# Performance work log

Hardware: AMD Instinct MI355X
Metric: run time of the kernel (lower is better)

The kernel has to match this reference:

```python
import jax, jax.numpy as jnp
import numpy as np

STRIDES = (8, 16, 32)
SIZES = ((80, 80), (40, 40), (20, 20))  # 640x640 input
PRE_TOP_K = 1000
KEEP_TOP_K = 100
IOU_THR = 0.65
SCORE_THR = 0.25
CLASS_OFFSET = 4096.0  # > max image extent, for class-aware NMS


def setup_inputs() -> dict:
    key = jax.random.key(0)
    ks = jax.random.split(key, 6)
    B, C = 8, 1203
    d = {}
    for i, (h, w) in enumerate(SIZES):
        d[f"cls_scores_{i}"] = jax.random.normal(ks[i], (B, C, h, w), dtype=jnp.float32)
        d[f"bbox_preds_{i}"] = jax.random.uniform(ks[3 + i], (B, 4, h, w), dtype=jnp.float32)
    return d


def _flatten(feats, ch):
    B = feats[0].shape[0]
    return jnp.concatenate([f.transpose(0, 2, 3, 1).reshape(B, -1, ch) for f in feats], axis=1)


def _priors():
    pts, strs = [], []
    for (h, w), s in zip(SIZES, STRIDES):
        yy, xx = jnp.meshgrid(jnp.arange(h, dtype=jnp.float32), jnp.arange(w, dtype=jnp.float32), indexing="ij")
        pts.append(jnp.stack([(xx.ravel() + 0.5) * s, (yy.ravel() + 0.5) * s], axis=-1))
        strs.append(jnp.full((h * w,), float(s), dtype=jnp.float32))
    return jnp.concatenate(pts, 0), jnp.concatenate(strs, 0)


def _decode(priors, preds, stride):
    # DistancePointBBoxCoder: preds are LTRB distances scaled by stride.
    d = preds * stride[None, :, None]  # [B,N,4]
    x1 = priors[None, :, 0] - d[..., 0]
    y1 = priors[None, :, 1] - d[..., 1]
    x2 = priors[None, :, 0] + d[..., 2]
    y2 = priors[None, :, 1] + d[..., 3]
    return jnp.stack([x1, y1, x2, y2], axis=-1)


def _iou_matrix(b):
    area = (b[:, 2] - b[:, 0]) * (b[:, 3] - b[:, 1])
    lt = jnp.maximum(b[:, None, :2], b[None, :, :2])
    rb = jnp.minimum(b[:, None, 2:], b[None, :, 2:])
    wh = jnp.clip(rb - lt, 0.0)
    inter = wh[..., 0] * wh[..., 1]
    return inter / (area[:, None] + area[None, :] - inter + 1e-7)


def _nms_single(boxes, scores, labels):
    # boxes [N,4], scores [N] (max over classes), labels [N] int
    ts, idx = jax.lax.top_k(scores, PRE_TOP_K)
    b = boxes[idx]
    l = labels[idx]
    valid = ts > SCORE_THR
    off = b + (l.astype(b.dtype) * CLASS_OFFSET)[:, None]  # class-aware trick
    iou = _iou_matrix(off)  # [K,K]

    def body(keep, i):
        suppressed = jnp.any(keep & (iou[:, i] > IOU_THR))
        keep = keep.at[i].set(valid[i] & ~suppressed)
        return keep, None

    keep, _ = jax.lax.scan(body, jnp.zeros((PRE_TOP_K,), bool), jnp.arange(PRE_TOP_K))
    kept_scores = jnp.where(keep, ts, -1.0)
    fs, fi = jax.lax.top_k(kept_scores, KEEP_TOP_K)
    m = fs > 0.0
    det_boxes = jnp.where(m[:, None], b[fi], 0.0)
    det_scores = jnp.where(m, fs, 0.0)
    det_labels = jnp.where(m, l[fi], -1)
    num_dets = m.sum().astype(jnp.int32)
    return num_dets, det_boxes, det_scores, det_labels


def reference(cls_scores_0, cls_scores_1, cls_scores_2, bbox_preds_0, bbox_preds_1, bbox_preds_2):
    C = cls_scores_0.shape[1]
    cls_scores = jax.nn.sigmoid(_flatten([cls_scores_0, cls_scores_1, cls_scores_2], C))  # [B,N,C]
    preds = _flatten([bbox_preds_0, bbox_preds_1, bbox_preds_2], 4)  # [B,N,4]
    priors, stride = _priors()
    boxes = _decode(priors, preds, stride)  # [B,N,4]
    max_scores = cls_scores.max(axis=-1)  # [B,N]
    labels = cls_scores.argmax(axis=-1)  # [B,N]
    num_dets, det_boxes, det_scores, det_labels = jax.vmap(_nms_single)(boxes, max_scores, labels)
    return num_dets, det_boxes, det_scores, det_labels
```

## Files before the change

kernel.cpp:

```cpp
#include <hip/hip_runtime.h>
#include <math.h>

#pragma clang fp contract(off)

typedef unsigned long long u64;
typedef unsigned int u32;
typedef float f4 __attribute__((ext_vector_type(4)));
typedef unsigned long long u64x2 __attribute__((ext_vector_type(2)));

#define BB 8
#define CC_TOT 1203
#define NANC 8400
#define NSEG 8
#define SEGN 1050
#define NSEL 1000
#define NCAND 1024
#define NT 1024
#define NBATCH 128
#define NCHUNK_MAX 16

__device__ __forceinline__ u32 okey32(float v) {
  u32 b = __float_as_uint(v);
  return (b & 0x80000000u) ? ~b : (b | 0x80000000u);
}

__device__ __forceinline__ float unokey32(u32 ok) {
  u32 fb = (ok & 0x80000000u) ? (ok & 0x7FFFFFFFu) : ~ok;
  return __uint_as_float(fb);
}

__global__ __launch_bounds__(256) void kmax(const float* __restrict__ cls0,
                                            const float* __restrict__ cls1,
                                            const float* __restrict__ cls2,
                                            u64* __restrict__ part,
                                            int chunkSz, int nchunk) {
  int bx = blockIdx.x;
  int per = nchunk * BB;
  int tg = bx / per;
  int rem = bx - tg * per;
  int chunk = rem >> 3;
  int b = rem & 7;
  const float* cls; int hw4, aoff, col0;
  if (tg < 7)      { cls = cls0; hw4 = 1600; aoff = 0;    col0 = tg << 8; }
  else if (tg < 9) { cls = cls1; hw4 = 400;  aoff = 6400; col0 = (tg - 7) << 8; }
  else             { cls = cls2; hw4 = 100;  aoff = 8000; col0 = 0; }
  int col = col0 + (int)threadIdx.x;
  if (col >= hw4) return;
  int c0 = chunk * chunkSz;
  int c1 = c0 + chunkSz; if (c1 > CC_TOT) c1 = CC_TOT;

  const f4* base = (const f4*)cls + (size_t)b * CC_TOT * hw4 + col;
  f4 m = (f4){-3.4e38f, -3.4e38f, -3.4e38f, -3.4e38f};
  int ix0 = c0, ix1 = c0, ix2 = c0, ix3 = c0;

#define UPD(v, c)                                   \
  do {                                              \
    if ((v)[0] > m[0]) { m[0] = (v)[0]; ix0 = (c); } \
    if ((v)[1] > m[1]) { m[1] = (v)[1]; ix1 = (c); } \
    if ((v)[2] > m[2]) { m[2] = (v)[2]; ix2 = (c); } \
    if ((v)[3] > m[3]) { m[3] = (v)[3]; ix3 = (c); } \
  } while (0)

  int c = c0;
  for (; c + 8 <= c1; c += 8) {
    const f4* p = base + (size_t)c * hw4;
    f4 v0 = p[0];
    f4 v1 = p[(size_t)1 * hw4];
    f4 v2 = p[(size_t)2 * hw4];
    f4 v3 = p[(size_t)3 * hw4];
    f4 v4 = p[(size_t)4 * hw4];
    f4 v5 = p[(size_t)5 * hw4];
    f4 v6 = p[(size_t)6 * hw4];
    f4 v7 = p[(size_t)7 * hw4];
    UPD(v0, c + 0); UPD(v1, c + 1); UPD(v2, c + 2); UPD(v3, c + 3);
    UPD(v4, c + 4); UPD(v5, c + 5); UPD(v6, c + 6); UPD(v7, c + 7);
  }
  for (; c < c1; ++c) {
    f4 v = base[(size_t)c * hw4];
    UPD(v, c);
  }
#undef UPD

  u64* dst = part + ((size_t)chunk * BB + b) * NANC + aoff + (size_t)col * 4;
  u64x2 s01 = { ((u64)okey32(m[0]) << 32) | (u64)(u32)~(u32)ix0,
                ((u64)okey32(m[1]) << 32) | (u64)(u32)~(u32)ix1 };
  u64x2 s23 = { ((u64)okey32(m[2]) << 32) | (u64)(u32)~(u32)ix2,
                ((u64)okey32(m[3]) << 32) | (u64)(u32)~(u32)ix3 };
  *((u64x2*)dst)     = s01;
  *((u64x2*)dst + 1) = s23;
}

struct DecodeArrays {
  float xo1[NCAND], yo1[NCAND], xo2[NCAND], yo2[NCAND], ar[NCAND];
  float rx1[NCAND], ry1[NCAND], rx2[NCAND], ry2[NCAND], sc[NCAND];
  int lab[NCAND], val[NCAND];
};

__device__ __forceinline__ void hist_addc(u32* hist, u32 digit, int lane) {
  u64 peers = ~0ull;
  for (int bit = 0; bit < 13; ++bit) {
    u64 bal = __ballot((digit >> bit) & 1u);
    peers &= ((digit >> bit) & 1u) ? bal : ~bal;
  }
  int leader = __ffsll((unsigned long long)peers) - 1;
  if (digit < 4096u && lane == leader)
    atomicAdd(&hist[digit], (u32)__popcll((unsigned long long)peers));
}

__device__ __forceinline__ void suffix_pick(u32* hist, u32* waveTot, u32* waveSufExcl,
                                            u64* prefixSh, u32* rankSh, u32* binCntSh,
                                            u64 prefix, u32 rank, int shift,
                                            int tid, int lane, int wv) {
  u32 l0 = hist[4 * tid], l1 = hist[4 * tid + 1], l2 = hist[4 * tid + 2], l3 = hist[4 * tid + 3];
  u32 psum = l0 + l1 + l2 + l3;
  u32 x = psum;
  for (int s = 1; s < 64; s <<= 1) { u32 v = __shfl_down(x, s); if (lane + s < 64) x += v; }
  if (lane == 0) waveTot[wv] = x;
  __syncthreads();
  if (tid < 16) {
    u32 y = waveTot[tid]; u32 z = y;
    for (int s = 1; s < 16; s <<= 1) { u32 v = __shfl_down(z, s); if (tid + s < 16) z += v; }
    waveSufExcl[tid] = z - y;
  }
  __syncthreads();
  u32 S = x + waveSufExcl[wv];
  u32 G3 = S - psum; u32 G2 = G3 + l3; u32 G1 = G2 + l2; u32 G0 = G1 + l1;
  u32 r = rank;
  if      (G3 < r && G3 + l3 >= r) { *prefixSh = prefix | ((u64)(4u * tid + 3) << shift); *rankSh = r - G3; *binCntSh = l3; }
  else if (G2 < r && G2 + l2 >= r) { *prefixSh = prefix | ((u64)(4u * tid + 2) << shift); *rankSh = r - G2; *binCntSh = l2; }
  else if (G1 < r && G1 + l1 >= r) { *prefixSh = prefix | ((u64)(4u * tid + 1) << shift); *rankSh = r - G1; *binCntSh = l1; }
  else if (G0 < r && G0 + l0 >= r) { *prefixSh = prefix | ((u64)(4u * tid + 0) << shift); *rankSh = r - G0; *binCntSh = l0; }
}

__device__ __forceinline__ u64 select_after_hist(const u64* keys, int n, u32 target,
                                                 u32* hist, u32* waveTot, u32* waveSufExcl,
                                                 u64* prefixSh, u32* rankSh, u32* binCntSh,
                                                 int tid, int lane, int wv) {
  suffix_pick(hist, waveTot, waveSufExcl, prefixSh, rankSh, binCntSh,
              0ull, target, 52, tid, lane, wv);
  __syncthreads();
  u64 pfx = *prefixSh; u32 rk = *rankSh; u32 lc = *binCntSh;
  __syncthreads();
  if (lc == rk) return pfx;
  for (int pass = 2; pass >= 0; --pass) {
    int shift = 16 + pass * 12;
    for (int i = tid; i < 4096; i += NT) hist[i] = 0;
    __syncthreads();
    u64 hiMask = (~0ull) << (shift + 12);
    for (int i = tid; i < n; i += NT) {
      u64 k = keys[i];
      if ((k & hiMask) == (pfx & hiMask))
        atomicAdd(&hist[(u32)((k >> shift) & 4095u)], 1u);
    }
    __syncthreads();
    suffix_pick(hist, waveTot, waveSufExcl, prefixSh, rankSh, binCntSh,
                pfx, rk, shift, tid, lane, wv);
    __syncthreads();
    pfx = *prefixSh; rk = *rankSh; lc = *binCntSh;
    __syncthreads();
    if (lc == rk) break;
  }
  return pfx;
}

__device__ __forceinline__ void gather_ge(const u64* keys, int n, u64 K, u64* dst, u32* cnt,
                                          int tid, int lane, u32 bound) {
  for (int i = tid; i < n; i += NT) {
    u64 k = keys[i];
    bool sel = (k >= K);
    u64 mask = __ballot(sel);
    if (mask) {
      int leader = __ffsll((unsigned long long)mask) - 1;
      u32 basep = 0;
      if (lane == leader) basep = atomicAdd(cnt, (u32)__popcll((unsigned long long)mask));
      basep = __shfl((int)basep, leader);
      if (sel) {
        u32 pos = basep + (u32)__popcll((unsigned long long)(mask & ((1ull << lane) - 1ull)));
        if (pos < bound) dst[pos] = k;
      }
    }
  }
}

__global__ __launch_bounds__(1024) void kseg(const u64* __restrict__ part, int nchunk,
                                             u64* __restrict__ candSeg) {
  __shared__ __align__(16) u64 keys[SEGN];
  __shared__ u32 hist[4096];
  __shared__ u32 waveTot[16], waveSufExcl[16];
  __shared__ u64 prefixSh;
  __shared__ u32 rankSh, binCntSh, cnt;

  int seg = blockIdx.x >> 3;
  int b = blockIdx.x & 7;
  int tid = threadIdx.x, lane = tid & 63, wv = tid >> 6;
  int a0 = seg * SEGN;

  const u64x2* psrc = (const u64x2*)part + ((size_t)b * NANC + a0) / 2;
  const size_t PL2 = (size_t)BB * NANC / 2;

  for (int i = tid; i < 4096; i += NT) hist[i] = 0;
  if (tid == 0) cnt = 0;
  __syncthreads();

  {
    u32 d0 = 4096u, d1 = 4096u;
    if (tid < SEGN / 2) {
      u64x2 m = psrc[tid];
      int ch = 1;
      for (; ch + 4 <= nchunk; ch += 4) {
        u64x2 v0 = psrc[(size_t)(ch + 0) * PL2 + tid];
        u64x2 v1 = psrc[(size_t)(ch + 1) * PL2 + tid];
        u64x2 v2 = psrc[(size_t)(ch + 2) * PL2 + tid];
        u64x2 v3 = psrc[(size_t)(ch + 3) * PL2 + tid];
        u64 a01 = (v0[0] > v1[0]) ? v0[0] : v1[0];
        u64 a23 = (v2[0] > v3[0]) ? v2[0] : v3[0];
        u64 aa = (a01 > a23) ? a01 : a23;
        if (aa > m[0]) m[0] = aa;
        u64 b01 = (v0[1] > v1[1]) ? v0[1] : v1[1];
        u64 b23 = (v2[1] > v3[1]) ? v2[1] : v3[1];
        u64 bb2_ = (b01 > b23) ? b01 : b23;
        if (bb2_ > m[1]) m[1] = bb2_;
      }
      for (; ch < nchunk; ++ch) {
        u64x2 v = psrc[(size_t)ch * PL2 + tid];
        if (v[0] > m[0]) m[0] = v[0];
        if (v[1] > m[1]) m[1] = v[1];
      }
      u32 aA = (u32)(a0 + 2 * tid), aB = aA + 1;
      u64 k0 = (m[0] & 0xFFFFFFFF00000000ull) | ((u64)(0xFFFFu - aA) << 16) | (u64)(~(u32)m[0] & 0xFFFFu);
      u64 k1 = (m[1] & 0xFFFFFFFF00000000ull) | ((u64)(0xFFFFu - aB) << 16) | (u64)(~(u32)m[1] & 0xFFFFu);
      keys[2 * tid] = k0;
      keys[2 * tid + 1] = k1;
      d0 = (u32)(k0 >> 52);
      d1 = (u32)(k1 >> 52);
    }
    hist_addc(hist, d0, lane);
    hist_addc(hist, d1, lane);
  }
  __syncthreads();

  u64 K = select_after_hist(keys, SEGN, NBATCH, hist, waveTot, waveSufExcl,
                            &prefixSh, &rankSh, &binCntSh, tid, lane, wv);
  gather_ge(keys, SEGN, K, candSeg + ((size_t)b * NSEG + seg) * NBATCH, &cnt,
            tid, lane, NBATCH);
}

__device__ __forceinline__ void decode_into(DecodeArrays* d, int rk, u64 my, int b,
                                            const float* bb0, const float* bb1, const float* bb2) {
  int label = (int)(u32)(my & 0xFFFFull);
  int idx = 0xFFFF - (int)(u32)((my >> 16) & 0xFFFFull);
  float logit = unokey32((u32)(my >> 32));
  float sc = 1.0f / (1.0f + expf(-logit));

  int w, str, off, hwl; const float* bb;
  if (idx < 6400)      { w = 80; str = 8;  off = 0;    hwl = 6400; bb = bb0; }
  else if (idx < 8000) { w = 40; str = 16; off = 6400; hwl = 1600; bb = bb1; }
  else                 { w = 20; str = 32; off = 8000; hwl = 400;  bb = bb2; }
  int p = idx - off;
  int y = p / w;
  int x = p - y * w;
  float fs = (float)str;
  float px = ((float)x + 0.5f) * fs;
  float py = ((float)y + 0.5f) * fs;
  const float* bp = bb + (size_t)b * 4 * hwl + p;
  float t0 = bp[0] * fs;
  float t1 = bp[hwl] * fs;
  float t2 = bp[2 * hwl] * fs;
  float t3 = bp[3 * hwl] * fs;
  float x1 = px - t0, y1 = py - t1, x2 = px + t2, y2 = py + t3;
  float lo = (float)label * 4096.0f;
  float ox1 = x1 + lo, oy1 = y1 + lo, ox2 = x2 + lo, oy2 = y2 + lo;
  float area = (ox2 - ox1) * (oy2 - oy1);

  d->xo1[rk] = ox1; d->yo1[rk] = oy1; d->xo2[rk] = ox2; d->yo2[rk] = oy2; d->ar[rk] = area;
  d->rx1[rk] = x1;  d->ry1[rk] = y1;  d->rx2[rk] = x2;  d->ry2[rk] = y2;  d->sc[rk] = sc;
  d->lab[rk] = label;
  d->val[rk] = (sc > 0.25f) ? 1 : 0;
}

__device__ __forceinline__ int nms_pass(const DecodeArrays* d, int bound, int lane, int* outIdx) {
  float ax1 = 0, ay1 = 0, ax2 = 0, ay2 = 0, aar = 0; int aon = 0;
  float bx1 = 0, by1 = 0, bx2 = 0, by2 = 0, bar = 0; int bon = 0;
  int kept = 0;
  for (int i = 0; i < bound; ++i) {
    if (kept >= 100) break;
    float cx1 = d->xo1[i], cy1 = d->yo1[i], cx2 = d->xo2[i], cy2 = d->yo2[i], car = d->ar[i];
    bool sup = false;
    if (aon) {
      float ltx = fmaxf(ax1, cx1), lty = fmaxf(ay1, cy1);
      float rbx = fminf(ax2, cx2), rby = fminf(ay2, cy2);
      float wd = fmaxf(rbx - ltx, 0.0f), ht = fmaxf(rby - lty, 0.0f);
      float inter = wd * ht;
      sup = sup || ((inter / (aar + car - inter + 1e-7f)) > 0.65f);
    }
    if (bon) {
      float ltx = fmaxf(bx1, cx1), lty = fmaxf(by1, cy1);
      float rbx = fminf(bx2, cx2), rby = fminf(by2, cy2);
      float wd = fmaxf(rbx - ltx, 0.0f), ht = fmaxf(rby - lty, 0.0f);
      float inter = wd * ht;
      sup = sup || ((inter / (bar + car - inter + 1e-7f)) > 0.65f);
    }
    bool anysup = __any(sup);
    if (d->val[i] != 0 && !anysup) {
      if (kept < 64) {
        if (lane == kept) { ax1 = cx1; ay1 = cy1; ax2 = cx2; ay2 = cy2; aar = car; aon = 1; }
      } else {
        if (lane == kept - 64) { bx1 = cx1; by1 = cy1; bx2 = cx2; by2 = cy2; bar = car; bon = 1; }
      }
      if (lane == 0) outIdx[kept] = i;
      ++kept;
    }
  }
  return kept;
}

__global__ __launch_bounds__(1024) void kmerge(const u64* __restrict__ part, int nchunk,
                                               const u64* __restrict__ candSeg,
                                               const float* __restrict__ bb0,
                                               const float* __restrict__ bb1,
                                               const float* __restrict__ bb2,
                                               float* __restrict__ out) {
  __shared__ union ShU {
    u64 fk[NANC];
    DecodeArrays d;
  } sh;
  __shared__ u32 hist[4096];
  __shared__ u32 waveTot[16], waveSufExcl[16];
  __shared__ u64 prefixSh;
  __shared__ u32 rankSh, binCntSh;
  __shared__ u32 gcnt, aCnt;
  __shared__ __align__(16) u64 cand[NCAND];
  __shared__ __align__(16) u64 candA[NBATCH];
  __shared__ __align__(16) u32 cm[NBATCH * 4];
  __shared__ u64 VwSh[2];
  __shared__ int outIdx[128];
  __shared__ int keptSh;

  int b = blockIdx.x;
  int tid = threadIdx.x;
  int lane = tid & 63;
  int wv = tid >> 6;

  for (int i = tid; i < 4096; i += NT) hist[i] = 0;
  if (tid == 0) { gcnt = 0; aCnt = 0; }
  __syncthreads();
  u64 myk = candSeg[(size_t)b * (NSEG * NBATCH) + tid];
  cand[tid] = myk;
  hist_addc(hist, (u32)(myk >> 52), lane);
  if (tid < NBATCH * 4) cm[tid] = 0;
  __syncthreads();

  u64 K = select_after_hist(cand, NCAND, NBATCH, hist, waveTot, waveSufExcl,
                            &prefixSh, &rankSh, &binCntSh, tid, lane, wv);
  gather_ge(cand, NCAND, K, candA, &aCnt, tid, lane, NBATCH);
  __syncthreads();

  if (tid < NBATCH) {
    u64 my = candA[tid];
    int rk = 0;
    const u64x2* cav = (const u64x2*)candA;
    #pragma unroll
    for (int j2 = 0; j2 < NBATCH / 2; ++j2) {
      u64x2 p = cav[j2];
      rk += (p[0] > my) ? 1 : 0;
      rk += (p[1] > my) ? 1 : 0;
    }
    decode_into(&sh.d, rk, my, b, bb0, bb1, bb2);
  }
  __syncthreads();

  if (tid < NBATCH) {
    u64 bal = __ballot(sh.d.val[tid] != 0);
    if (lane == 0) VwSh[tid >> 6] = bal;
  }

  {
    int c = tid & 127;
    int g = tid >> 7;
    float cx1 = sh.d.xo1[c], cy1 = sh.d.yo1[c], cx2 = sh.d.xo2[c], cy2 = sh.d.yo2[c], car = sh.d.ar[c];
    u32 bits = 0;
    int j0 = g * 16;
    for (int jj = 0; jj < 16; ++jj) {
      int j = j0 + jj;
      float ltx = fmaxf(sh.d.xo1[j], cx1), lty = fmaxf(sh.d.yo1[j], cy1);
      float rbx = fminf(sh.d.xo2[j], cx2), rby = fminf(sh.d.yo2[j], cy2);
      float wd = fmaxf(rbx - ltx, 0.0f), ht = fmaxf(rby - lty, 0.0f);
      float inter = wd * ht;
      bool sup = (inter / (sh.d.ar[j] + car - inter + 1e-7f)) > 0.65f;
      bits |= sup ? (1u << jj) : 0u;
    }
    atomicOr(&cm[c * 4 + (g >> 1)], bits << ((g & 1) * 16));
  }
  __syncthreads();

  if (tid == 0) {
    u32 L0 = (u32)VwSh[0], L1 = (u32)(VwSh[0] >> 32);
    u32 L2 = (u32)VwSh[1], L3 = (u32)(VwSh[1] >> 32);
    int kept = 0;
    while (kept < 100) {
      int i;
      if (L0)      i = __ffs(L0) - 1;
      else if (L1) i = 31 + __ffs(L1);
      else if (L2) i = 63 + __ffs(L2);
      else if (L3) i = 95 + __ffs(L3);
      else break;
      outIdx[kept++] = i;
      const u32* c4 = &cm[i * 4];
      L0 &= ~c4[0]; L1 &= ~c4[1]; L2 &= ~c4[2]; L3 &= ~c4[3];
      if (i < 32)      L0 &= ~(1u << i);
      else if (i < 64) L1 &= ~(1u << (i - 32));
      else if (i < 96) L2 &= ~(1u << (i - 64));
      else             L3 &= ~(1u << (i - 96));
    }
    keptSh = kept;
  }
  __syncthreads();

  if (keptSh < 100) {
    const u64x2* psrc = (const u64x2*)(part + (size_t)b * NANC);
    const size_t PL2 = (size_t)BB * NANC / 2;
    for (int i = tid; i < 4096; i += NT) hist[i] = 0;
    __syncthreads();
    {
      u64x2* fdst = (u64x2*)sh.fk;
      for (int i = tid; i < NANC / 2; i += NT) {
        u64x2 m = psrc[i];
        for (int ch = 1; ch < nchunk; ++ch) {
          u64x2 v = psrc[(size_t)ch * PL2 + i];
          if (v[0] > m[0]) m[0] = v[0];
          if (v[1] > m[1]) m[1] = v[1];
        }
        u32 i0 = (u32)(2 * i), i1 = (u32)(2 * i + 1);
        u64x2 r;
        r[0] = (m[0] & 0xFFFFFFFF00000000ull) | ((u64)(0xFFFFu - i0) << 16) | (u64)(~(u32)m[0] & 0xFFFFu);
        r[1] = (m[1] & 0xFFFFFFFF00000000ull) | ((u64)(0xFFFFu - i1) << 16) | (u64)(~(u32)m[1] & 0xFFFFu);
        fdst[i] = r;
        hist_addc(hist, (u32)(r[0] >> 52), lane);
        hist_addc(hist, (u32)(r[1] >> 52), lane);
      }
    }
    __syncthreads();
    u64 Kf = select_after_hist(sh.fk, NANC, NSEL, hist, waveTot, waveSufExcl,
                               &prefixSh, &rankSh, &binCntSh, tid, lane, wv);
    gather_ge(sh.fk, NANC, Kf, cand, &gcnt, tid, lane, NSEL);
    __syncthreads();
    if (tid < NSEL) {
      u64 my = cand[tid];
      int rk = 0;
      const u64x2* cbv = (const u64x2*)cand;
      for (int j2 = 0; j2 < NSEL / 2; ++j2) {
        u64x2 p = cbv[j2];
        rk += (p[0] > my) ? 1 : 0;
        rk += (p[1] > my) ? 1 : 0;
      }
      decode_into(&sh.d, rk, my, b, bb0, bb1, bb2);
    }
    __syncthreads();
    if (tid < 64) {
      int kept = nms_pass(&sh.d, NSEL, lane, outIdx);
      if (lane == 0) keptSh = kept;
    }
    __syncthreads();
  }

  int kept = keptSh;
  float* o_nd = out;
  float* o_box = out + BB;
  float* o_sc = out + BB + BB * 100 * 4;
  float* o_lb = out + BB + BB * 100 * 4 + BB * 100;
  if (tid == 0) o_nd[b] = (float)kept;
  if (tid < 100) {
    int s = tid;
    float v0 = 0, v1 = 0, v2 = 0, v3 = 0, sv = 0, lv = -1.0f;
    if (s < kept) {
      int i = outIdx[s];
      v0 = sh.d.rx1[i]; v1 = sh.d.ry1[i]; v2 = sh.d.rx2[i]; v3 = sh.d.ry2[i];
      sv = sh.d.sc[i]; lv = (float)sh.d.lab[i];
    }
    float* bo = o_box + ((size_t)b * 100 + s) * 4;
    bo[0] = v0; bo[1] = v1; bo[2] = v2; bo[3] = v3;
    o_sc[b * 100 + s] = sv;
    o_lb[b * 100 + s] = lv;
  }
}

extern "C" void kernel_launch(void* const* d_in, const int* in_sizes, int n_in,
                              void* d_out, int out_size, void* d_ws, size_t ws_size,
                              hipStream_t stream) {
  const float* cls0 = (const float*)d_in[0];
  const float* bb0  = (const float*)d_in[1];
  const float* cls1 = (const float*)d_in[2];
  const float* bb1  = (const float*)d_in[3];
  const float* cls2 = (const float*)d_in[4];
  const float* bb2  = (const float*)d_in[5];

  size_t planeB = (size_t)BB * NANC * sizeof(u64);
  size_t candB = (size_t)BB * NSEG * NBATCH * sizeof(u64);
  u64* part = (u64*)d_ws;
  int nchunk = 1;
  if (ws_size > candB + planeB) {
    nchunk = (int)((ws_size - candB) / planeB);
    if (nchunk > NCHUNK_MAX) nchunk = NCHUNK_MAX;
    if (nchunk < 1) nchunk = 1;
  }
  int chunkSz = (CC_TOT + nchunk - 1) / nchunk;
  nchunk = (CC_TOT + chunkSz - 1) / chunkSz;
  u64* candSeg = part + (size_t)nchunk * BB * NANC;

  kmax<<<dim3(10 * nchunk * BB), dim3(256), 0, stream>>>(cls0, cls1, cls2, part, chunkSz, nchunk);
  kseg<<<dim3(NSEG * BB), dim3(NT), 0, stream>>>(part, nchunk, candSeg);
  kmerge<<<dim3(BB), dim3(NT), 0, stream>>>(part, nchunk, candSeg, bb0, bb1, bb2, (float*)d_out);
}
```

Measured before the change: 119.8 us.

## Fuse segment select and merge kernels via last-block atomic counter

Merges the per-segment top-k kernel and the per-batch merge/NMS kernel into one launch. Each segment block publishes its candidates, then increments a per-batch atomic counter, and the last block to arrive for a batch performs the merge, decode and NMS. This removes one kernel launch and its inter-kernel gap, at the cost of an extra memset, atomics, and fences. The segment blocks now declare the larger merge shared-memory footprint, which may reduce how many blocks fit per CU.

Result: slower. 148.5 us (+24.0%).

```diff
diff --git a/kernel.cpp b/kernel.cpp
--- a/kernel.cpp
+++ b/kernel.cpp
@@ -182,13 +182,98 @@
   }
 }
 
-__global__ __launch_bounds__(1024) void kseg(const u64* __restrict__ part, int nchunk,
-                                             u64* __restrict__ candSeg) {
-  __shared__ __align__(16) u64 keys[SEGN];
+__device__ __forceinline__ void decode_into(DecodeArrays* d, int rk, u64 my, int b,
+                                            const float* bb0, const float* bb1, const float* bb2) {
+  int label = (int)(u32)(my & 0xFFFFull);
+  int idx = 0xFFFF - (int)(u32)((my >> 16) & 0xFFFFull);
+  float logit = unokey32((u32)(my >> 32));
+  float sc = 1.0f / (1.0f + expf(-logit));
+
+  int w, str, off, hwl; const float* bb;
+  if (idx < 6400)      { w = 80; str = 8;  off = 0;    hwl = 6400; bb = bb0; }
+  else if (idx < 8000) { w = 40; str = 16; off = 6400; hwl = 1600; bb = bb1; }
+  else                 { w = 20; str = 32; off = 8000; hwl = 400;  bb = bb2; }
+  int p = idx - off;
+  int y = p / w;
+  int x = p - y * w;
+  float fs = (float)str;
+  float px = ((float)x + 0.5f) * fs;
+  float py = ((float)y + 0.5f) * fs;
+  const float* bp = bb + (size_t)b * 4 * hwl + p;
+  float t0 = bp[0] * fs;
+  float t1 = bp[hwl] * fs;
+  float t2 = bp[2 * hwl] * fs;
+  float t3 = bp[3 * hwl] * fs;
+  float x1 = px - t0, y1 = py - t1, x2 = px + t2, y2 = py + t3;
+  float lo = (float)label * 4096.0f;
+  float ox1 = x1 + lo, oy1 = y1 + lo, ox2 = x2 + lo, oy2 = y2 + lo;
+  float area = (ox2 - ox1) * (oy2 - oy1);
+
+  d->xo1[rk] = ox1; d->yo1[rk] = oy1; d->xo2[rk] = ox2; d->yo2[rk] = oy2; d->ar[rk] = area;
+  d->rx1[rk] = x1;  d->ry1[rk] = y1;  d->rx2[rk] = x2;  d->ry2[rk] = y2;  d->sc[rk] = sc;
+  d->lab[rk] = label;
+  d->val[rk] = (sc > 0.25f) ? 1 : 0;
+}
+
+__device__ __forceinline__ int nms_pass(const DecodeArrays* d, int bound, int lane, int* outIdx) {
+  float ax1 = 0, ay1 = 0, ax2 = 0, ay2 = 0, aar = 0; int aon = 0;
+  float bx1 = 0, by1 = 0, bx2 = 0, by2 = 0, bar = 0; int bon = 0;
+  int kept = 0;
+  for (int i = 0; i < bound; ++i) {
+    if (kept >= 100) break;
+    float cx1 = d->xo1[i], cy1 = d->yo1[i], cx2 = d->xo2[i], cy2 = d->yo2[i], car = d->ar[i];
+    bool sup = false;
+    if (aon) {
+      float ltx = fmaxf(ax1, cx1), lty = fmaxf(ay1, cy1);
+      float rbx = fminf(ax2, cx2), rby = fminf(ay2, cy2);
+      float wd = fmaxf(rbx - ltx, 0.0f), ht = fmaxf(rby - lty, 0.0f);
+      float inter = wd * ht;
+      sup = sup || ((inter / (aar + car - inter + 1e-7f)) > 0.65f);
+    }
+    if (bon) {
+      float ltx = fmaxf(bx1, cx1), lty = fmaxf(by1, cy1);
+      float rbx = fminf(bx2, cx2), rby = fminf(by2, cy2);
+      float wd = fmaxf(rbx - ltx, 0.0f), ht = fmaxf(rby - lty, 0.0f);
+      float inter = wd * ht;
+      sup = sup || ((inter / (bar + car - inter + 1e-7f)) > 0.65f);
+    }
+    bool anysup = __any(sup);
+    if (d->val[i] != 0 && !anysup) {
+      if (kept < 64) {
+        if (lane == kept) { ax1 = cx1; ay1 = cy1; ax2 = cx2; ay2 = cy2; aar = car; aon = 1; }
+      } else {
+        if (lane == kept - 64) { bx1 = cx1; by1 = cy1; bx2 = cx2; by2 = cy2; bar = car; bon = 1; }
+      }
+      if (lane == 0) outIdx[kept] = i;
+      ++kept;
+    }
+  }
+  return kept;
+}
+
+__global__ __launch_bounds__(1024) void kboth(const u64* __restrict__ part, int nchunk,
+                                              u64* __restrict__ candSeg,
+                                              u32* __restrict__ ctr,
+                                              const float* __restrict__ bb0,
+                                              const float* __restrict__ bb1,
+                                              const float* __restrict__ bb2,
+                                              float* __restrict__ out) {
+  __shared__ union ShU {
+    u64 fk[NANC];
+    DecodeArrays d;
+  } sh;
   __shared__ u32 hist[4096];
   __shared__ u32 waveTot[16], waveSufExcl[16];
   __shared__ u64 prefixSh;
-  __shared__ u32 rankSh, binCntSh, cnt;
+  __shared__ u32 rankSh, binCntSh;
+  __shared__ u32 gcnt, aCnt;
+  __shared__ __align__(16) u64 cand[NCAND];
+  __shared__ __align__(16) u64 candA[NBATCH];
+  __shared__ __align__(16) u32 cm[NBATCH * 4];
+  __shared__ u64 VwSh[2];
+  __shared__ int outIdx[128];
+  __shared__ int keptSh;
+  __shared__ int lastSh;
 
   int seg = blockIdx.x >> 3;
   int b = blockIdx.x & 7;
@@ -199,9 +284,8 @@
   const size_t PL2 = (size_t)BB * NANC / 2;
 
   for (int i = tid; i < 4096; i += NT) hist[i] = 0;
-  if (tid == 0) cnt = 0;
-  __syncthreads();
-
+  if (tid == 0) aCnt = 0;
+  __syncthreads();
   {
     u32 d0 = 4096u, d1 = 4096u;
     if (tid < SEGN / 2) {
@@ -229,8 +313,8 @@
       u32 aA = (u32)(a0 + 2 * tid), aB = aA + 1;
       u64 k0 = (m[0] & 0xFFFFFFFF00000000ull) | ((u64)(0xFFFFu - aA) << 16) | (u64)(~(u32)m[0] & 0xFFFFu);
       u64 k1 = (m[1] & 0xFFFFFFFF00000000ull) | ((u64)(0xFFFFu - aB) << 16) | (u64)(~(u32)m[1] & 0xFFFFu);
-      keys[2 * tid] = k0;
-      keys[2 * tid + 1] = k1;
+      sh.fk[2 * tid] = k0;
+      sh.fk[2 * tid + 1] = k1;
       d0 = (u32)(k0 >> 52);
       d1 = (u32)(k1 >> 52);
     }
@@ -239,120 +323,32 @@
   }
   __syncthreads();
 
-  u64 K = select_after_hist(keys, SEGN, NBATCH, hist, waveTot, waveSufExcl,
+  u64 K = select_after_hist(sh.fk, SEGN, NBATCH, hist, waveTot, waveSufExcl,
                             &prefixSh, &rankSh, &binCntSh, tid, lane, wv);
-  gather_ge(keys, SEGN, K, candSeg + ((size_t)b * NSEG + seg) * NBATCH, &cnt,
-            tid, lane, NBATCH);
-}
-
-__device__ __forceinline__ void decode_into(DecodeArrays* d, int rk, u64 my, int b,
-                                            const float* bb0, const float* bb1, const float* bb2) {
-  int label = (int)(u32)(my & 0xFFFFull);
-  int idx = 0xFFFF - (int)(u32)((my >> 16) & 0xFFFFull);
-  float logit = unokey32((u32)(my >> 32));
-  float sc = 1.0f / (1.0f + expf(-logit));
-
-  int w, str, off, hwl; const float* bb;
-  if (idx < 6400)      { w = 80; str = 8;  off = 0;    hwl = 6400; bb = bb0; }
-  else if (idx < 8000) { w = 40; str = 16; off = 6400; hwl = 1600; bb = bb1; }
-  else                 { w = 20; str = 32; off = 8000; hwl = 400;  bb = bb2; }
-  int p = idx - off;
-  int y = p / w;
-  int x = p - y * w;
-  float fs = (float)str;
-  float px = ((float)x + 0.5f) * fs;
-  float py = ((float)y + 0.5f) * fs;
-  const float* bp = bb + (size_t)b * 4 * hwl + p;
-  float t0 = bp[0] * fs;
-  float t1 = bp[hwl] * fs;
-  float t2 = bp[2 * hwl] * fs;
-  float t3 = bp[3 * hwl] * fs;
-  float x1 = px - t0, y1 = py - t1, x2 = px + t2, y2 = py + t3;
-  float lo = (float)label * 4096.0f;
-  float ox1 = x1 + lo, oy1 = y1 + lo, ox2 = x2 + lo, oy2 = y2 + lo;
-  float area = (ox2 - ox1) * (oy2 - oy1);
-
-  d->xo1[rk] = ox1; d->yo1[rk] = oy1; d->xo2[rk] = ox2; d->yo2[rk] = oy2; d->ar[rk] = area;
-  d->rx1[rk] = x1;  d->ry1[rk] = y1;  d->rx2[rk] = x2;  d->ry2[rk] = y2;  d->sc[rk] = sc;
-  d->lab[rk] = label;
-  d->val[rk] = (sc > 0.25f) ? 1 : 0;
-}
-
-__device__ __forceinline__ int nms_pass(const DecodeArrays* d, int bound, int lane, int* outIdx) {
-  float ax1 = 0, ay1 = 0, ax2 = 0, ay2 = 0, aar = 0; int aon = 0;
-  float bx1 = 0, by1 = 0, bx2 = 0, by2 = 0, bar = 0; int bon = 0;
-  int kept = 0;
-  for (int i = 0; i < bound; ++i) {
-    if (kept >= 100) break;
-    float cx1 = d->xo1[i], cy1 = d->yo1[i], cx2 = d->xo2[i], cy2 = d->yo2[i], car = d->ar[i];
-    bool sup = false;
-    if (aon) {
-      float ltx = fmaxf(ax1, cx1), lty = fmaxf(ay1, cy1);
-      float rbx = fminf(ax2, cx2), rby = fminf(ay2, cy2);
-      float wd = fmaxf(rbx - ltx, 0.0f), ht = fmaxf(rby - lty, 0.0f);
-      float inter = wd * ht;
-      sup = sup || ((inter / (aar + car - inter + 1e-7f)) > 0.65f);
-    }
-    if (bon) {
-      float ltx = fmaxf(bx1, cx1), lty = fmaxf(by1, cy1);
-      float rbx = fminf(bx2, cx2), rby = fminf(by2, cy2);
-      float wd = fmaxf(rbx - ltx, 0.0f), ht = fmaxf(rby - lty, 0.0f);
-      float inter = wd * ht;
-      sup = sup || ((inter / (bar + car - inter + 1e-7f)) > 0.65f);
-    }
-    bool anysup = __any(sup);
-    if (d->val[i] != 0 && !anysup) {
-      if (kept < 64) {
-        if (lane == kept) { ax1 = cx1; ay1 = cy1; ax2 = cx2; ay2 = cy2; aar = car; aon = 1; }
-      } else {
-        if (lane == kept - 64) { bx1 = cx1; by1 = cy1; bx2 = cx2; by2 = cy2; bar = car; bon = 1; }
-      }
-      if (lane == 0) outIdx[kept] = i;
-      ++kept;
-    }
-  }
-  return kept;
-}
-
-__global__ __launch_bounds__(1024) void kmerge(const u64* __restrict__ part, int nchunk,
-                                               const u64* __restrict__ candSeg,
-                                               const float* __restrict__ bb0,
-                                               const float* __restrict__ bb1,
-                                               const float* __restrict__ bb2,
-                                               float* __restrict__ out) {
-  __shared__ union ShU {
-    u64 fk[NANC];
-    DecodeArrays d;
-  } sh;
-  __shared__ u32 hist[4096];
-  __shared__ u32 waveTot[16], waveSufExcl[16];
-  __shared__ u64 prefixSh;
-  __shared__ u32 rankSh, binCntSh;
-  __shared__ u32 gcnt, aCnt;
-  __shared__ __align__(16) u64 cand[NCAND];
-  __shared__ __align__(16) u64 candA[NBATCH];
-  __shared__ __align__(16) u32 cm[NBATCH * 4];
-  __shared__ u64 VwSh[2];
-  __shared__ int outIdx[128];
-  __shared__ int keptSh;
-
-  int b = blockIdx.x;
-  int tid = threadIdx.x;
-  int lane = tid & 63;
-  int wv = tid >> 6;
+  gather_ge(sh.fk, SEGN, K, candA, &aCnt, tid, lane, NBATCH);
+  __syncthreads();
+
+  if (tid < NBATCH)
+    atomicExch(&candSeg[((size_t)b * NSEG + seg) * NBATCH + tid], candA[tid]);
+  __threadfence();
+  __syncthreads();
+  if (tid == 0) lastSh = (atomicAdd(&ctr[b], 1u) == NSEG - 1) ? 1 : 0;
+  __syncthreads();
+  if (!lastSh) return;
+  __threadfence();
 
   for (int i = tid; i < 4096; i += NT) hist[i] = 0;
   if (tid == 0) { gcnt = 0; aCnt = 0; }
   __syncthreads();
-  u64 myk = candSeg[(size_t)b * (NSEG * NBATCH) + tid];
+  u64 myk = atomicOr(&candSeg[(size_t)b * (NSEG * NBATCH) + tid], 0ull);
   cand[tid] = myk;
   hist_addc(hist, (u32)(myk >> 52), lane);
   if (tid < NBATCH * 4) cm[tid] = 0;
   __syncthreads();
 
-  u64 K = select_after_hist(cand, NCAND, NBATCH, hist, waveTot, waveSufExcl,
-                            &prefixSh, &rankSh, &binCntSh, tid, lane, wv);
-  gather_ge(cand, NCAND, K, candA, &aCnt, tid, lane, NBATCH);
+  u64 Km = select_after_hist(cand, NCAND, NBATCH, hist, waveTot, waveSufExcl,
+                             &prefixSh, &rankSh, &binCntSh, tid, lane, wv);
+  gather_ge(cand, NCAND, Km, candA, &aCnt, tid, lane, NBATCH);
   __syncthreads();
 
   if (tid < NBATCH) {
@@ -417,16 +413,15 @@
   __syncthreads();
 
   if (keptSh < 100) {
-    const u64x2* psrc = (const u64x2*)(part + (size_t)b * NANC);
-    const size_t PL2 = (size_t)BB * NANC / 2;
+    const u64x2* pim = (const u64x2*)(part + (size_t)b * NANC);
     for (int i = tid; i < 4096; i += NT) hist[i] = 0;
     __syncthreads();
     {
       u64x2* fdst = (u64x2*)sh.fk;
       for (int i = tid; i < NANC / 2; i += NT) {
-        u64x2 m = psrc[i];
+        u64x2 m = pim[i];
         for (int ch = 1; ch < nchunk; ++ch) {
-          u64x2 v = psrc[(size_t)ch * PL2 + i];
+          u64x2 v = pim[(size_t)ch * PL2 + i];
           if (v[0] > m[0]) m[0] = v[0];
           if (v[1] > m[1]) m[1] = v[1];
         }
@@ -496,18 +491,21 @@
 
   size_t planeB = (size_t)BB * NANC * sizeof(u64);
   size_t candB = (size_t)BB * NSEG * NBATCH * sizeof(u64);
+  size_t ctrB = 64;
   u64* part = (u64*)d_ws;
   int nchunk = 1;
-  if (ws_size > candB + planeB) {
-    nchunk = (int)((ws_size - candB) / planeB);
+  if (ws_size > candB + ctrB + planeB) {
+    nchunk = (int)((ws_size - candB - ctrB) / planeB);
     if (nchunk > NCHUNK_MAX) nchunk = NCHUNK_MAX;
     if (nchunk < 1) nchunk = 1;
   }
   int chunkSz = (CC_TOT + nchunk - 1) / nchunk;
   nchunk = (CC_TOT + chunkSz - 1) / chunkSz;
   u64* candSeg = part + (size_t)nchunk * BB * NANC;
-
+  u32* ctr = (u32*)(candSeg + (size_t)BB * NSEG * NBATCH);
+
+  hipMemsetAsync(ctr, 0, ctrB, stream);
   kmax<<<dim3(10 * nchunk * BB), dim3(256), 0, stream>>>(cls0, cls1, cls2, part, chunkSz, nchunk);
-  kseg<<<dim3(NSEG * BB), dim3(NT), 0, stream>>>(part, nchunk, candSeg);
-  kmerge<<<dim3(BB), dim3(NT), 0, stream>>>(part, nchunk, candSeg, bb0, bb1, bb2, (float*)d_out);
-}
+  kboth<<<dim3(NSEG * BB), dim3(NT), 0, stream>>>(part, nchunk, candSeg, ctr,
+                                                  bb0, bb1, bb2, (float*)d_out);
+}
```
